# Kernel optimization log

Hardware: AMD Instinct MI355X
Metric: run time of the kernel (lower is better)

The kernel has to match this reference:

```python
import jax, jax.numpy as jnp
import numpy as np

B, T, NN = 128, 128, 8          # batch, time_window, nodes per graph (hardcoded in source)
N = B * T * NN                  # 131072 flattened node rows
F_IN, C = 32, 64                # node_features, spatial_features
E = 1_048_576                   # edges (avg degree 8)
EPS = 1e-5


def _gcn(x, src, dst, W, b):
    # PyG GCNConv: h = D^{-1/2}(A+I)D^{-1/2} X W + b, self-loops added, symmetric norm
    h = x @ W                                           # [N, C]
    loop = jnp.arange(N, dtype=src.dtype)
    s = jnp.concatenate([src, loop])
    d = jnp.concatenate([dst, loop])
    deg = jax.ops.segment_sum(jnp.ones_like(s, dtype=h.dtype), d, num_segments=N)
    dinv = jax.lax.rsqrt(deg)                           # deg >= 1 due to self loops
    msg = h[s] * (dinv[s] * dinv[d])[:, None]           # gather + scale
    out = jax.ops.segment_sum(msg, d, num_segments=N)   # scatter-add
    return out + b


def _conv2d(x, w, b, pad_w):
    y = jax.lax.conv_general_dilated(
        x, w, window_strides=(1, 1), padding=[(0, 0), (pad_w, pad_w)],
        dimension_numbers=("NCHW", "OIHW", "NCHW"))
    return y + b[None, :, None, None]


def _bn_relu(x, g, beta):
    # BatchNorm2d in training mode: batch statistics, biased variance
    mu = x.mean(axis=(0, 2, 3), keepdims=True)
    var = x.var(axis=(0, 2, 3), keepdims=True)
    y = (x - mu) * jax.lax.rsqrt(var + EPS)
    return jax.nn.relu(y * g[None, :, None, None] + beta[None, :, None, None])


def _layer(x, src, dst, gw, gb, tw, tb, bg, bb, ow, ob):
    h = _gcn(x, src, dst, gw, gb)                       # [N, C]
    h = h.reshape(B, T, NN, -1).transpose(0, 3, 2, 1)   # [B, C, NN, T]
    h = _conv2d(h, tw, tb, 1)                           # (1,3) temporal conv, pad (0,1)
    h = _bn_relu(h, bg, bb)
    h = _conv2d(h, ow, ob, 0)                           # 1x1 conv (squeeze() is a no-op here)
    h = jnp.tanh(h)
    return h.reshape(-1, h.shape[1])                    # faithful to x.view(-1, x.shape[1])


def setup_inputs() -> dict:
    key = jax.random.key(0)
    ks = jax.random.split(key, 20)
    p = lambda k, shape: (jax.random.normal(k, shape, jnp.float32) * 0.05)
    inp = {
        "x": jax.random.normal(ks[0], (N, F_IN), jnp.float32),
        "edge_index": jax.random.randint(ks[1], (2, E), 0, N, jnp.int32),
        "gcn1_w": p(ks[2], (F_IN, C)), "gcn1_b": jnp.zeros((C,), jnp.float32),
        "t1_w": p(ks[3], (C, C, 1, 3)), "t1_b": jnp.zeros((C,), jnp.float32),
        "bn1_g": jnp.ones((C,), jnp.float32), "bn1_b": jnp.zeros((C,), jnp.float32),
        "o1_w": p(ks[4], (C, C, 1, 1)), "o1_b": jnp.zeros((C,), jnp.float32),
        "gcn2_w": p(ks[5], (C, C)), "gcn2_b": jnp.zeros((C,), jnp.float32),
        "t2_w": p(ks[6], (C, C, 1, 3)), "t2_b": jnp.zeros((C,), jnp.float32),
        "bn2_g": jnp.ones((C,), jnp.float32), "bn2_b": jnp.zeros((C,), jnp.float32),
        "o2_w": p(ks[7], (C, C, 1, 1)), "o2_b": jnp.zeros((C,), jnp.float32),
        "reg_w": p(ks[8], (C, 8)), "reg_b": jnp.zeros((8,), jnp.float32),
    }
    return inp


def reference(x, edge_index, gcn1_w, gcn1_b, t1_w, t1_b, bn1_g, bn1_b, o1_w, o1_b,
              gcn2_w, gcn2_b, t2_w, t2_b, bn2_g, bn2_b, o2_w, o2_b, reg_w, reg_b):
    src, dst = edge_index[0], edge_index[1]
    h = _layer(x, src, dst, gcn1_w, gcn1_b, t1_w, t1_b, bn1_g, bn1_b, o1_w, o1_b)
    h = _layer(h, src, dst, gcn2_w, gcn2_b, t2_w, t2_b, bn2_g, bn2_b, o2_w, o2_b)
    h = h @ reg_w + reg_b                                # [N, 8]
    h = h.reshape(B, T, NN, -1)
    return h.mean(axis=(1, 3))                           # [B, NN] = [128, 8]
```

## Files before the change

kernel.cpp:

```cpp
#include <hip/hip_runtime.h>
#include <stdint.h>

typedef unsigned short u16;
typedef __attribute__((ext_vector_type(8))) short bf16x8;
typedef __attribute__((ext_vector_type(4))) float f32x4;

static const int N_NODES = 131072;
static const int N_EDGES = 1048576;

__device__ __forceinline__ float u2f(u16 u){
  union{uint32_t i; float f;} w; w.i = ((uint32_t)u)<<16; return w.f;
}
__device__ __forceinline__ u16 f2u(float f){
  union{float f; uint32_t u;} v; v.f=f;
  uint32_t u=v.u;
  u += 0x7fff + ((u>>16)&1);
  return (u16)(u>>16);
}
__device__ __forceinline__ float bits2f(uint32_t b){
  union{uint32_t i; float f;} w; w.i = b; return w.f;
}
__device__ __forceinline__ float ldmix(const void* p, int i, int isbf){
  return isbf ? u2f(((const u16*)p)[i]) : ((const float*)p)[i];
}
__device__ __forceinline__ float ftanh(float x){
  float ax = fabsf(x);
  float e  = __expf(ax + ax);
  float r  = 1.f - __fdividef(2.f, e + 1.f);
  return copysignf(r, x);
}

__global__ __launch_bounds__(256) void k_hist(const int* __restrict__ dst, int* __restrict__ H,
                                              const uint32_t* __restrict__ x, int* __restrict__ flag,
                                              float* __restrict__ stats1, float* __restrict__ stats2,
                                              float* __restrict__ zacc){
  __shared__ int h[256];
  __shared__ int dcnt;
  int tid = threadIdx.x;
  h[tid] = 0;
  if (blockIdx.x == 0){
    if (tid == 0) dcnt = 0;
    for (int i=tid; i<512; i+=256){ stats1[i] = 0.f; stats2[i] = 0.f; }
    for (int i=tid; i<1024; i+=256) zacc[i] = 0.f;
  }
  __syncthreads();
  if (blockIdx.x == 0){
    uint32_t e = (x[tid]>>7) & 0xFFu;
    int ok = (e >= 0x6Fu && e <= 0x85u) ? 1 : 0;
    unsigned long long m = __ballot(ok);
    if ((tid & 63) == 0) atomicAdd(&dcnt, (int)__popcll(m));
    __syncthreads();
    if (tid == 0) *flag = (dcnt >= 128) ? 1 : 0;
  }
  int base = blockIdx.x*4096;
  #pragma unroll
  for (int i=0;i<16;i++){
    int e2 = base + i*256 + tid;
    atomicAdd(&h[(dst[e2] & (N_NODES-1))>>9], 1);
  }
  __syncthreads();
  H[blockIdx.x*256 + tid] = h[tid];
}

__device__ __forceinline__ void wcomb_one(int Kin, const void* gW, const void* gb, const void* tw,
                                          int isbf, u16* Wtb, float* braw, int r, int co){
  if (r < 3*Kin){
    int k = r / Kin, j = r - (r/Kin)*Kin;
    float acc = 0.f;
    for (int c=0; c<64; c++)
      acc += ldmix(gW, j*64+c, isbf) * ldmix(tw, co*192 + c*3 + k, isbf);
    Wtb[co*(3*Kin) + r] = f2u(acc);
  } else {
    int k = r - 3*Kin;
    float acc = 0.f;
    for (int c=0; c<64; c++)
      acc += ldmix(gb, c, isbf) * ldmix(tw, co*192 + c*3 + k, isbf);
    braw[k*64 + co] = acc;
  }
}

__global__ __launch_bounds__(256) void k_colscan_w(const int* __restrict__ H, int* __restrict__ P,
                                                   int* __restrict__ bt,
                                                   const void* __restrict__ g1w, const void* __restrict__ g1b,
                                                   const void* __restrict__ t1w,
                                                   const void* __restrict__ g2w, const void* __restrict__ g2b,
                                                   const void* __restrict__ t2w,
                                                   const void* __restrict__ o1w, const void* __restrict__ o2w,
                                                   const int* __restrict__ flag,
                                                   u16* __restrict__ Wtb1, float* __restrict__ braw1,
                                                   u16* __restrict__ Wtb2, float* __restrict__ braw2,
                                                   u16* __restrict__ owb1, u16* __restrict__ owb2){
  int tid = threadIdx.x;
  if (blockIdx.x < 256){
    __shared__ int sc[256];
    int b = blockIdx.x;
    int v = H[tid*256 + b];
    sc[tid] = v; __syncthreads();
    for (int d=1; d<256; d<<=1){
      int o = (tid>=d) ? sc[tid-d] : 0; __syncthreads();
      sc[tid] += o; __syncthreads();
    }
    P[tid*256 + b] = sc[tid] - v;
    if (tid==255) bt[b] = sc[255];
  } else {
    int isbf = *flag;
    int r = (blockIdx.x - 256)*4 + (tid>>6);
    int co = tid & 63;
    if (r >= 422) return;
    if (r < 99) wcomb_one(32, g1w, g1b, t1w, isbf, Wtb1, braw1, r, co);
    else if (r < 294) wcomb_one(64, g2w, g2b, t2w, isbf, Wtb2, braw2, r-99, co);
    else if (r < 358){
      int row = r - 294;
      owb1[row*64 + co] = f2u(ldmix(o1w, row*64 + co, isbf));
    } else {
      int row = r - 358;
      owb2[row*64 + co] = f2u(ldmix(o2w, row*64 + co, isbf));
    }
  }
}

__global__ __launch_bounds__(256) void k_scatter2(const int* __restrict__ src, const int* __restrict__ dst,
                                                  const int* __restrict__ P, const int* __restrict__ bt,
                                                  uint32_t* __restrict__ ebuf){
  __shared__ int cu[256], sc[256];
  int tid = threadIdx.x;
  int v = bt[tid];
  sc[tid] = v; __syncthreads();
  for (int d=1; d<256; d<<=1){
    int o = (tid>=d) ? sc[tid-d] : 0; __syncthreads();
    sc[tid] += o; __syncthreads();
  }
  cu[tid] = (sc[tid] - v) + P[blockIdx.x*256 + tid];
  __syncthreads();
  int base = blockIdx.x*4096;
  #pragma unroll
  for (int i=0;i<16;i++){
    int e = base + i*256 + tid;
    int s = src[e] & (N_NODES-1);
    int d = dst[e] & (N_NODES-1);
    int pos = atomicAdd(&cu[d>>9], 1);
    ebuf[pos] = (uint32_t)s | ((uint32_t)(d & 511) << 17);
  }
}

__global__ __launch_bounds__(512) void k_bsort2(const uint32_t* __restrict__ ebuf, const int* __restrict__ bt,
                                                const void* __restrict__ x, const int* __restrict__ flag,
                                                int* __restrict__ adj, int* __restrict__ offs,
                                                int* __restrict__ deg, float* __restrict__ dinv,
                                                u16* __restrict__ Bout, int* __restrict__ perm){
  __shared__ uint32_t ein[5120], outs[5120];
  __shared__ int hist[512], sc[512], cu[512];
  __shared__ int sct[256];
  __shared__ float dv[512];
  __shared__ int dh2[64], dsc[64];
  int b = blockIdx.x, tid = threadIdx.x;
  if (tid < 256){ sct[tid] = bt[tid]; }
  __syncthreads();
  for (int d=1; d<256; d<<=1){
    int o = (tid < 256 && tid>=d) ? sct[tid-d] : 0; __syncthreads();
    if (tid < 256) sct[tid] += o; __syncthreads();
  }
  int lo = sct[b] - bt[b], hi = sct[b];
  int cnt = hi - lo; if (cnt > 5120) cnt = 5120; if (cnt < 0) cnt = 0;
  hist[tid] = 0;
  __syncthreads();
  for (int i=tid; i<cnt; i+=512){
    uint32_t p = ebuf[lo+i];
    ein[i] = p;
    atomicAdd(&hist[(p>>17)&511], 1);
  }
  __syncthreads();
  sc[tid] = hist[tid];
  __syncthreads();
  for (int d=1; d<512; d<<=1){
    int v = (tid>=d) ? sc[tid-d] : 0;
    __syncthreads();
    sc[tid] += v;
    __syncthreads();
  }
  {
    int ex = sc[tid] - hist[tid];
    int node = b*512 + tid;
    offs[node] = lo + ex;
    deg[node]  = hist[tid];
    float rs = rsqrtf((float)hist[tid] + 1.0f);
    dinv[node] = rs;
    dv[tid] = rs;
    cu[tid] = ex;
  }
  __syncthreads();
  for (int i=tid; i<cnt; i+=512){
    uint32_t p = ein[i];
    int pos = atomicAdd(&cu[(p>>17)&511], 1);
    outs[pos] = p & 0x1FFFFu;
  }
  __syncthreads();
  if (tid < 64) dh2[tid] = 0;
  __syncthreads();
  int mybin = min(hist[tid], 63);
  atomicAdd(&dh2[mybin], 1);
  __syncthreads();
  if (tid == 0){
    int s = 0;
    for (int i=0;i<64;i++){ int c = dh2[i]; dsc[i] = s; s += c; }
  }
  __syncthreads();
  {
    int rank = atomicAdd(&dsc[mybin], 1);
    perm[(b<<9) + rank] = (b<<9) + tid;
  }
  for (int i=tid; i<cnt; i+=512) adj[lo+i] = (int)outs[i];
  int isbf = *flag;
  {
    uint32_t* Bd = (uint32_t*)Bout;
    for (int u=tid; u<8192; u+=512){
      int nl = u>>4, jd = u&15;
      int half = ((b<<9) + nl)*16 + jd;
      float x0, x1;
      if (isbf){
        uint32_t pr = ((const uint32_t*)x)[half];
        x0 = bits2f(pr<<16); x1 = bits2f(pr & 0xFFFF0000u);
      } else {
        float2 f2 = ((const float2*)x)[half];
        x0 = f2.x; x1 = f2.y;
      }
      float d = dv[nl];
      Bd[half] = (uint32_t)f2u(x0*d) | ((uint32_t)f2u(x1*d) << 16);
    }
  }
}

__device__ __forceinline__ void acc16(uint4 a, float* acc){
  acc[0] += bits2f(a.x<<16); acc[1] += bits2f(a.x&0xFFFF0000u);
  acc[2] += bits2f(a.y<<16); acc[3] += bits2f(a.y&0xFFFF0000u);
  acc[4] += bits2f(a.z<<16); acc[5] += bits2f(a.z&0xFFFF0000u);
  acc[6] += bits2f(a.w<<16); acc[7] += bits2f(a.w&0xFFFF0000u);
}
template<int F>
__global__ __launch_bounds__(256) void k_aggp2(const u16* __restrict__ Xs, const int* __restrict__ perm,
                                               const int* __restrict__ adj, const int* __restrict__ offs,
                                               const int* __restrict__ deg, const float* __restrict__ dinv,
                                               u16* __restrict__ out){
  constexpr int CH  = F/8;
  constexpr int GPW = 64/CH;
  int tid = threadIdx.x;
  int wv = tid>>6, lane = tid&63;
  int g = lane / CH;
  int k = lane % CH;
  int n = perm[blockIdx.x*(4*GPW) + wv*GPW + g];
  int o = offs[n] & (N_EDGES-1);
  int cnt = min(deg[n], 8192);
  const uint4* X4 = (const uint4*)Xs;
  uint4 sv = X4[(size_t)n*CH + k];
  float acc[8] = {0,0,0,0,0,0,0,0};
  acc16(sv, acc);
  int e = 0;
  for (; e+8 <= cnt; e += 8){
    int i0 = adj[o+e+0] & (N_NODES-1);
    int i1 = adj[o+e+1] & (N_NODES-1);
    int i2 = adj[o+e+2] & (N_NODES-1);
    int i3 = adj[o+e+3] & (N_NODES-1);
    int i4 = adj[o+e+4] & (N_NODES-1);
    int i5 = adj[o+e+5] & (N_NODES-1);
    int i6 = adj[o+e+6] & (N_NODES-1);
    int i7 = adj[o+e+7] & (N_NODES-1);
    uint4 a0 = X4[(size_t)i0*CH + k];
    uint4 a1 = X4[(size_t)i1*CH + k];
    uint4 a2 = X4[(size_t)i2*CH + k];
    uint4 a3 = X4[(size_t)i3*CH + k];
    uint4 a4 = X4[(size_t)i4*CH + k];
    uint4 a5 = X4[(size_t)i5*CH + k];
    uint4 a6 = X4[(size_t)i6*CH + k];
    uint4 a7 = X4[(size_t)i7*CH + k];
    acc16(a0, acc); acc16(a1, acc); acc16(a2, acc); acc16(a3, acc);
    acc16(a4, acc); acc16(a5, acc); acc16(a6, acc); acc16(a7, acc);
  }
  if (e+4 <= cnt){
    int i0 = adj[o+e+0] & (N_NODES-1);
    int i1 = adj[o+e+1] & (N_NODES-1);
    int i2 = adj[o+e+2] & (N_NODES-1);
    int i3 = adj[o+e+3] & (N_NODES-1);
    uint4 a0 = X4[(size_t)i0*CH + k];
    uint4 a1 = X4[(size_t)i1*CH + k];
    uint4 a2 = X4[(size_t)i2*CH + k];
    uint4 a3 = X4[(size_t)i3*CH + k];
    acc16(a0, acc); acc16(a1, acc); acc16(a2, acc); acc16(a3, acc);
    e += 4;
  }
  for (; e < cnt; e++){
    int s = adj[o+e] & (N_NODES-1);
    uint4 a = X4[(size_t)s*CH + k];
    acc16(a, acc);
  }
  float dv = dinv[n];
  uint4 r;
  r.x = (uint32_t)f2u(acc[0]*dv) | ((uint32_t)f2u(acc[1]*dv) << 16);
  r.y = (uint32_t)f2u(acc[2]*dv) | ((uint32_t)f2u(acc[3]*dv) << 16);
  r.z = (uint32_t)f2u(acc[4]*dv) | ((uint32_t)f2u(acc[5]*dv) << 16);
  r.w = (uint32_t)f2u(acc[6]*dv) | ((uint32_t)f2u(acc[7]*dv) << 16);
  ((uint4*)out)[(size_t)n*CH + k] = r;
}

template<int Kin>
__global__ __launch_bounds__(256) void k_tconv3(const u16* __restrict__ A, const u16* __restrict__ Wtb,
                                                const float* __restrict__ braw, const void* __restrict__ tb,
                                                const int* __restrict__ flag, u16* __restrict__ out,
                                                float* __restrict__ stats){
  constexpr int K  = 3*Kin;
  constexpr int SA = Kin + 8;
  constexpr int JH = Kin/2;
  constexpr int JL = (Kin==64) ? 5 : 4;
  __shared__ alignas(16) u16 At[66*SA];
  __shared__ float ball[64], bs0[64], bs2[64];
  __shared__ float wsum[4][64], wsum2[4][64];

  int isbf = *flag;
  int bid = blockIdx.x;
  int b = bid>>4, rem = bid&15, v = rem>>1, th = rem&1;
  const int tid = threadIdx.x;

  if (tid < 64){
    float b0=braw[tid], b1=braw[64+tid], b2=braw[128+tid];
    ball[tid] = ldmix(tb, tid, isbf) + b0 + b1 + b2;
    bs0[tid] = b0; bs2[tid] = b2;
  }
  {
    uint32_t* Ad = (uint32_t*)At;
    const uint32_t* Ag = (const uint32_t*)A;
    for (int u=tid; u<66*JH; u+=256){
      int ls = u >> JL, jd = u & (JH-1);
      int t = th*64 + ls - 1;
      uint32_t pack = 0;
      if (t >= 0 && t < 128)
        pack = Ag[((((b*128+t)*8+v))*Kin >> 1) + jd];
      Ad[ls*(SA/2) + jd] = pack;
    }
  }
  __syncthreads();

  int wv_ = tid >> 6, lane = tid & 63;
  int q = lane >> 4, l16 = lane & 15;
  int ltb0 = wv_ * 16;

  f32x4 acc[4];
  #pragma unroll
  for (int nt=0; nt<4; nt++) acc[nt] = (f32x4){0.f,0.f,0.f,0.f};

  #pragma unroll
  for (int s=0; s<K/32; s++){
    int kk = (32*s)/Kin;
    int j0 = 32*s - kk*Kin;
    int col = j0 + q*8;
    bf16x8 afr = *(const bf16x8*)&At[(ltb0 + l16 + kk)*SA + col];
    bf16x8 bfr[4];
    #pragma unroll
    for (int nt=0; nt<4; nt++){
      int co = nt*16 + l16;
      bfr[nt] = *(const bf16x8*)&Wtb[co*K + 32*s + q*8];
    }
    #pragma unroll
    for (int nt=0; nt<4; nt++)
      acc[nt] = __builtin_amdgcn_mfma_f32_16x16x32_bf16(afr, bfr[nt], acc[nt], 0, 0, 0);
  }

  float ls_[4] = {0,0,0,0}, ls2_[4] = {0,0,0,0};
  #pragma unroll
  for (int r=0; r<4; r++){
    int t = th*64 + ltb0 + q*4 + r;
    int base = (((b*128+t)*8+v)) << 6;
    #pragma unroll
    for (int nt=0; nt<4; nt++){
      int co = nt*16 + l16;
      float val = acc[nt][r] + ball[co];
      if (t == 0)   val -= bs0[co];
      if (t == 127) val -= bs2[co];
      out[base + co] = f2u(val);
      ls_[nt] += val; ls2_[nt] += val*val;
    }
  }
  #pragma unroll
  for (int nt=0; nt<4; nt++){
    ls_[nt]  += __shfl_xor(ls_[nt], 16);  ls_[nt]  += __shfl_xor(ls_[nt], 32);
    ls2_[nt] += __shfl_xor(ls2_[nt], 16); ls2_[nt] += __shfl_xor(ls2_[nt], 32);
  }
  if (q == 0){
    #pragma unroll
    for (int nt=0; nt<4; nt++){
      wsum[wv_][nt*16 + l16]  = ls_[nt];
      wsum2[wv_][nt*16 + l16] = ls2_[nt];
    }
  }
  __syncthreads();
  if (tid < 64){
    float a = wsum[0][tid]+wsum[1][tid]+wsum[2][tid]+wsum[3][tid];
    float a2 = wsum2[0][tid]+wsum2[1][tid]+wsum2[2][tid]+wsum2[3][tid];
    int bank = (bid & 3) * 128;
    atomicAdd(&stats[bank + tid], a);
    atomicAdd(&stats[bank + 64 + tid], a2);
  }
}

template<bool FINAL>
__global__ __launch_bounds__(256) void k_bnfuse3(const u16* __restrict__ X, const float* __restrict__ stats,
                                                 const void* __restrict__ gam, const void* __restrict__ bet,
                                                 const u16* __restrict__ owb, const void* __restrict__ ob,
                                                 const int* __restrict__ flag, const float* __restrict__ presc,
                                                 u16* __restrict__ out16,
                                                 float* __restrict__ zacc, const void* __restrict__ rw){
  constexpr int SA = 72;
  __shared__ alignas(16) u16 Yl[64*SA];
  __shared__ float kk[64], bsh[64], obs[64];
  __shared__ float rw_s[64];
  __shared__ float wred[4];
  int isbf = *flag;
  int bid = blockIdx.x;
  int b = bid>>4, rem = bid&15, v = rem>>1, th = rem&1;
  const int tid = threadIdx.x;
  const float invM = 1.0f/131072.0f;

  if (tid < 64){
    int ci = tid;
    float s1 = stats[ci] + stats[128+ci] + stats[256+ci] + stats[384+ci];
    float s2 = stats[64+ci] + stats[192+ci] + stats[320+ci] + stats[448+ci];
    float mu = s1*invM;
    float var = s2*invM - mu*mu;
    float rs = rsqrtf(fmaxf(var, 0.f) + 1e-5f);
    float kv = rs*ldmix(gam, ci, isbf);
    kk[ci] = kv;
    bsh[ci] = ldmix(bet, ci, isbf) - mu*kv;
    obs[ci] = ldmix(ob, ci, isbf);
    if (FINAL){
      float s = 0.f;
      #pragma unroll
      for (int f=0; f<8; f++) s += ldmix(rw, ci*8 + f, isbf);
      rw_s[ci] = s;
    }
  }
  __syncthreads();
  {
    uint32_t* Yd = (uint32_t*)Yl;
    const uint32_t* Xg = (const uint32_t*)X;
    for (int u=tid; u<64*32; u+=256){
      int lt = u>>5, jd = u&31;
      int ci = jd<<1;
      int t = th*64 + lt;
      int rowbase = (((b*128+t)*8+v)) << 6;
      uint32_t pr = Xg[(rowbase>>1) + jd];
      float x0 = bits2f(pr<<16);
      float x1 = bits2f(pr & 0xFFFF0000u);
      float y0 = fmaxf(x0*kk[ci] + bsh[ci], 0.f);
      float y1 = fmaxf(x1*kk[ci+1] + bsh[ci+1], 0.f);
      Yd[lt*(SA/2) + jd] = (uint32_t)f2u(y0) | ((uint32_t)f2u(y1) << 16);
    }
  }
  __syncthreads();

  int wv_ = tid >> 6, lane = tid & 63;
  int q = lane >> 4, l16 = lane & 15;
  int ltb0 = wv_ * 16;

  f32x4 acc[4];
  #pragma unroll
  for (int nt=0; nt<4; nt++) acc[nt] = (f32x4){0.f,0.f,0.f,0.f};

  #pragma unroll
  for (int s=0; s<2; s++){
    int col = 32*s + q*8;
    bf16x8 afr = *(const bf16x8*)&Yl[(ltb0 + l16)*SA + col];
    bf16x8 bfr[4];
    #pragma unroll
    for (int nt=0; nt<4; nt++){
      int co = nt*16 + l16;
      bfr[nt] = *(const bf16x8*)&owb[co*64 + col];
    }
    #pragma unroll
    for (int nt=0; nt<4; nt++)
      acc[nt] = __builtin_amdgcn_mfma_f32_16x16x32_bf16(afr, bfr[nt], acc[nt], 0, 0, 0);
  }

  __syncthreads();
  #pragma unroll
  for (int r=0; r<4; r++){
    int lt = ltb0 + q*4 + r;
    #pragma unroll
    for (int nt=0; nt<4; nt++){
      int co = nt*16 + l16;
      Yl[lt*SA + co] = f2u(acc[nt][r] + obs[co]);
    }
  }
  __syncthreads();
  if (!FINAL){
    for (int u=tid; u<4096; u+=256){
      int l = u & 63;
      int co = u >> 6;
      float z = ftanh(u2f(Yl[l*SA + co]));
      int r = (b<<10) + (co<<4) + (v<<1) + th;
      if (presc) z *= presc[r];
      out16[(r<<6) + l] = f2u(z);
    }
  } else {
    float zsum = 0.f;
    for (int u=tid; u<4096; u+=256){
      int l = u & 63;
      int co = u >> 6;
      float z = ftanh(u2f(Yl[l*SA + co]));
      zsum += z * rw_s[l];
    }
    for (int off=32; off; off>>=1) zsum += __shfl_down(zsum, off);
    if (lane == 0) wred[wv_] = zsum;
    __syncthreads();
    if (tid == 0){
      int base = (b<<3) + ((v&3)<<1) + th;
      atomicAdd(&zacc[base], wred[0] + wred[1] + wred[2] + wred[3]);
    }
  }
}

__global__ __launch_bounds__(256) void k_fin2(const float* __restrict__ zacc, const void* __restrict__ rb,
                                              const int* __restrict__ flag, void* __restrict__ out){
  int i = blockIdx.x*256 + threadIdx.x;
  if (i >= 1024) return;
  int isbf = *flag;
  float rbs = 0.f;
  #pragma unroll
  for (int f=0; f<8; f++) rbs += ldmix(rb, f, isbf);
  float val = zacc[i]*(1.0f/1024.0f) + rbs*0.125f;
  if (isbf) ((u16*)out)[i] = f2u(val);
  else      ((float*)out)[i] = val;
}

extern "C" void kernel_launch(void* const* d_in, const int* in_sizes, int n_in,
                              void* d_out, int out_size, void* d_ws, size_t ws_size,
                              hipStream_t stream){
  (void)in_sizes; (void)n_in; (void)out_size; (void)ws_size;
  char* p = (char*)d_ws;
  auto alloc = [&](size_t bytes){ void* r = (void*)p; p += (bytes + 255) & ~(size_t)255; return r; };
  u16*   U1   = (u16*)  alloc(sizeof(u16)*(size_t)N_NODES*64);
  u16*   U2   = (u16*)  alloc(sizeof(u16)*(size_t)N_NODES*64);
  u16*   C16  = (u16*)  alloc(sizeof(u16)*(size_t)N_NODES*64);
  int*   deg  = (int*)  alloc(sizeof(int)*N_NODES);
  float* dinv = (float*)alloc(sizeof(float)*N_NODES);
  int*   offs = (int*)  alloc(sizeof(int)*N_NODES);
  int*   adj  = (int*)  alloc(sizeof(int)*N_EDGES);
  int*   perm = (int*)  alloc(sizeof(int)*N_NODES);
  int*   H    = (int*)  alloc(sizeof(int)*256*256);
  int*   P    = (int*)  alloc(sizeof(int)*256*256);
  int*   bt   = (int*)  alloc(sizeof(int)*256);
  float* stats1=(float*)alloc(sizeof(float)*512);
  float* stats2=(float*)alloc(sizeof(float)*512);
  int*   flag = (int*)  alloc(sizeof(int)*64);
  u16*   Wtb1 = (u16*)  alloc(sizeof(u16)*96*64);
  float* braw1= (float*)alloc(sizeof(float)*192);
  u16*   Wtb2 = (u16*)  alloc(sizeof(u16)*192*64);
  float* braw2= (float*)alloc(sizeof(float)*192);
  u16*   owb1 = (u16*)  alloc(sizeof(u16)*64*64);
  u16*   owb2 = (u16*)  alloc(sizeof(u16)*64*64);
  float* zacc = (float*)alloc(sizeof(float)*1024);
  uint32_t* ebuf = (uint32_t*)C16;
  u16* Bs16 = U1;
  u16* A16  = U1 + (size_t)N_NODES*32;
  u16* D16  = U1;
  u16* E16  = U2;

  const void* x   = d_in[0];
  const int* edge = (const int*)d_in[1];
  const void* g1w = d_in[2];  const void* g1b = d_in[3];
  const void* t1w = d_in[4];  const void* t1b = d_in[5];
  const void* bn1g= d_in[6];  const void* bn1b= d_in[7];
  const void* o1w = d_in[8];  const void* o1b = d_in[9];
  const void* g2w = d_in[10]; const void* g2b = d_in[11];
  const void* t2w = d_in[12]; const void* t2b = d_in[13];
  const void* bn2g= d_in[14]; const void* bn2b= d_in[15];
  const void* o2w = d_in[16]; const void* o2b = d_in[17];
  const void* rw  = d_in[18]; const void* rb  = d_in[19];
  const int* src = edge;
  const int* dst = edge + N_EDGES;

  k_hist     <<<256, 256, 0, stream>>>(dst, H, (const uint32_t*)x, flag, stats1, stats2, zacc);
  k_colscan_w<<<362, 256, 0, stream>>>(H, P, bt, g1w, g1b, t1w, g2w, g2b, t2w, o1w, o2w, flag,
                                       Wtb1, braw1, Wtb2, braw2, owb1, owb2);
  k_scatter2 <<<256, 256, 0, stream>>>(src, dst, P, bt, ebuf);
  k_bsort2   <<<256, 512, 0, stream>>>(ebuf, bt, x, flag, adj, offs, deg, dinv, Bs16, perm);

  k_aggp2<32>  <<<N_NODES/64, 256, 0, stream>>>(Bs16, perm, adj, offs, deg, dinv, A16);
  k_tconv3<32> <<<2048, 256, 0, stream>>>(A16, Wtb1, braw1, t1b, flag, C16, stats1);
  k_bnfuse3<false><<<2048, 256, 0, stream>>>(C16, stats1, bn1g, bn1b, owb1, o1b, flag, dinv, D16,
                                             (float*)nullptr, (const void*)nullptr);

  k_aggp2<64>  <<<N_NODES/32, 256, 0, stream>>>(D16, perm, adj, offs, deg, dinv, E16);
  k_tconv3<64> <<<2048, 256, 0, stream>>>(E16, Wtb2, braw2, t2b, flag, C16, stats2);
  k_bnfuse3<true><<<2048, 256, 0, stream>>>(C16, stats2, bn2g, bn2b, owb2, o2b, flag, (const float*)nullptr,
                                            (u16*)nullptr, zacc, rw);
  k_fin2<<<4, 256, 0, stream>>>(zacc, rb, flag, d_out);
}
```

Before: 296.3 us.

## Fuse GCN neighbor aggregation into temporal conv kernel and drop degree-sorted permutation

The separate sparse aggregation kernel is removed. Each temporal-conv block now gathers and aggregates its own 66 time rows (64 plus a halo) straight into shared memory before the MFMA conv. This avoids writing the aggregated features to global memory and reading them back, and it removes the degree-binned node permutation built in the sort kernel. In exchange, the 2 halo rows per block are aggregated twice, and load balancing across lanes with different degrees is lost because nodes are no longer grouped by degree.

```diff
diff --git a/kernel.cpp b/kernel.cpp
--- a/kernel.cpp
+++ b/kernel.cpp
@@ -147,12 +147,11 @@
                                                 const void* __restrict__ x, const int* __restrict__ flag,
                                                 int* __restrict__ adj, int* __restrict__ offs,
                                                 int* __restrict__ deg, float* __restrict__ dinv,
-                                                u16* __restrict__ Bout, int* __restrict__ perm){
+                                                u16* __restrict__ Bout){
   __shared__ uint32_t ein[5120], outs[5120];
   __shared__ int hist[512], sc[512], cu[512];
   __shared__ int sct[256];
   __shared__ float dv[512];
-  __shared__ int dh2[64], dsc[64];
   int b = blockIdx.x, tid = threadIdx.x;
   if (tid < 256){ sct[tid] = bt[tid]; }
   __syncthreads();
@@ -195,20 +194,6 @@
     outs[pos] = p & 0x1FFFFu;
   }
   __syncthreads();
-  if (tid < 64) dh2[tid] = 0;
-  __syncthreads();
-  int mybin = min(hist[tid], 63);
-  atomicAdd(&dh2[mybin], 1);
-  __syncthreads();
-  if (tid == 0){
-    int s = 0;
-    for (int i=0;i<64;i++){ int c = dh2[i]; dsc[i] = s; s += c; }
-  }
-  __syncthreads();
-  {
-    int rank = atomicAdd(&dsc[mybin], 1);
-    perm[(b<<9) + rank] = (b<<9) + tid;
-  }
   for (int i=tid; i<cnt; i+=512) adj[lo+i] = (int)outs[i];
   int isbf = *flag;
   {
@@ -236,80 +221,17 @@
   acc[4] += bits2f(a.z<<16); acc[5] += bits2f(a.z&0xFFFF0000u);
   acc[6] += bits2f(a.w<<16); acc[7] += bits2f(a.w&0xFFFF0000u);
 }
-template<int F>
-__global__ __launch_bounds__(256) void k_aggp2(const u16* __restrict__ Xs, const int* __restrict__ perm,
-                                               const int* __restrict__ adj, const int* __restrict__ offs,
-                                               const int* __restrict__ deg, const float* __restrict__ dinv,
-                                               u16* __restrict__ out){
-  constexpr int CH  = F/8;
+
+template<int Kin>
+__global__ __launch_bounds__(256) void k_gconv(
+    const u16* __restrict__ Xs, const int* __restrict__ adj, const int* __restrict__ offs,
+    const int* __restrict__ deg, const float* __restrict__ dinv,
+    const u16* __restrict__ Wtb, const float* __restrict__ braw, const void* __restrict__ tb,
+    const int* __restrict__ flag, u16* __restrict__ out, float* __restrict__ stats){
+  constexpr int K   = 3*Kin;
+  constexpr int SA  = Kin + 8;
+  constexpr int CH  = Kin/8;
   constexpr int GPW = 64/CH;
-  int tid = threadIdx.x;
-  int wv = tid>>6, lane = tid&63;
-  int g = lane / CH;
-  int k = lane % CH;
-  int n = perm[blockIdx.x*(4*GPW) + wv*GPW + g];
-  int o = offs[n] & (N_EDGES-1);
-  int cnt = min(deg[n], 8192);
-  const uint4* X4 = (const uint4*)Xs;
-  uint4 sv = X4[(size_t)n*CH + k];
-  float acc[8] = {0,0,0,0,0,0,0,0};
-  acc16(sv, acc);
-  int e = 0;
-  for (; e+8 <= cnt; e += 8){
-    int i0 = adj[o+e+0] & (N_NODES-1);
-    int i1 = adj[o+e+1] & (N_NODES-1);
-    int i2 = adj[o+e+2] & (N_NODES-1);
-    int i3 = adj[o+e+3] & (N_NODES-1);
-    int i4 = adj[o+e+4] & (N_NODES-1);
-    int i5 = adj[o+e+5] & (N_NODES-1);
-    int i6 = adj[o+e+6] & (N_NODES-1);
-    int i7 = adj[o+e+7] & (N_NODES-1);
-    uint4 a0 = X4[(size_t)i0*CH + k];
-    uint4 a1 = X4[(size_t)i1*CH + k];
-    uint4 a2 = X4[(size_t)i2*CH + k];
-    uint4 a3 = X4[(size_t)i3*CH + k];
-    uint4 a4 = X4[(size_t)i4*CH + k];
-    uint4 a5 = X4[(size_t)i5*CH + k];
-    uint4 a6 = X4[(size_t)i6*CH + k];
-    uint4 a7 = X4[(size_t)i7*CH + k];
-    acc16(a0, acc); acc16(a1, acc); acc16(a2, acc); acc16(a3, acc);
-    acc16(a4, acc); acc16(a5, acc); acc16(a6, acc); acc16(a7, acc);
-  }
-  if (e+4 <= cnt){
-    int i0 = adj[o+e+0] & (N_NODES-1);
-    int i1 = adj[o+e+1] & (N_NODES-1);
-    int i2 = adj[o+e+2] & (N_NODES-1);
-    int i3 = adj[o+e+3] & (N_NODES-1);
-    uint4 a0 = X4[(size_t)i0*CH + k];
-    uint4 a1 = X4[(size_t)i1*CH + k];
-    uint4 a2 = X4[(size_t)i2*CH + k];
-    uint4 a3 = X4[(size_t)i3*CH + k];
-    acc16(a0, acc); acc16(a1, acc); acc16(a2, acc); acc16(a3, acc);
-    e += 4;
-  }
-  for (; e < cnt; e++){
-    int s = adj[o+e] & (N_NODES-1);
-    uint4 a = X4[(size_t)s*CH + k];
-    acc16(a, acc);
-  }
-  float dv = dinv[n];
-  uint4 r;
-  r.x = (uint32_t)f2u(acc[0]*dv) | ((uint32_t)f2u(acc[1]*dv) << 16);
-  r.y = (uint32_t)f2u(acc[2]*dv) | ((uint32_t)f2u(acc[3]*dv) << 16);
-  r.z = (uint32_t)f2u(acc[4]*dv) | ((uint32_t)f2u(acc[5]*dv) << 16);
-  r.w = (uint32_t)f2u(acc[6]*dv) | ((uint32_t)f2u(acc[7]*dv) << 16);
-  ((uint4*)out)[(size_t)n*CH + k] = r;
-}
-
-template<int Kin>
-__global__ __launch_bounds__(256) void k_tconv3(const u16* __restrict__ A, const u16* __restrict__ Wtb,
-                                                const float* __restrict__ braw, const void* __restrict__ tb,
-                                                const int* __restrict__ flag, u16* __restrict__ out,
-                                                float* __restrict__ stats){
-  constexpr int K  = 3*Kin;
-  constexpr int SA = Kin + 8;
-  constexpr int JH = Kin/2;
-  constexpr int JL = (Kin==64) ? 5 : 4;
   __shared__ alignas(16) u16 At[66*SA];
   __shared__ float ball[64], bs0[64], bs2[64];
   __shared__ float wsum[4][64], wsum2[4][64];
@@ -318,40 +240,84 @@
   int bid = blockIdx.x;
   int b = bid>>4, rem = bid&15, v = rem>>1, th = rem&1;
   const int tid = threadIdx.x;
+  int wv_ = tid >> 6, lane = tid & 63;
+  int q = lane >> 4, l16 = lane & 15;
+  int ltb0 = wv_ * 16;
+  int g = lane / CH, kch = lane % CH;
+  const uint4* X4 = (const uint4*)Xs;
 
   if (tid < 64){
     float b0=braw[tid], b1=braw[64+tid], b2=braw[128+tid];
     ball[tid] = ldmix(tb, tid, isbf) + b0 + b1 + b2;
     bs0[tid] = b0; bs2[tid] = b2;
   }
-  {
-    uint32_t* Ad = (uint32_t*)At;
-    const uint32_t* Ag = (const uint32_t*)A;
-    for (int u=tid; u<66*JH; u+=256){
-      int ls = u >> JL, jd = u & (JH-1);
-      int t = th*64 + ls - 1;
-      uint32_t pack = 0;
-      if (t >= 0 && t < 128)
-        pack = Ag[((((b*128+t)*8+v))*Kin >> 1) + jd];
-      Ad[ls*(SA/2) + jd] = pack;
-    }
-  }
-  __syncthreads();
-
-  int wv_ = tid >> 6, lane = tid & 63;
-  int q = lane >> 4, l16 = lane & 15;
-  int ltb0 = wv_ * 16;
-
-  f32x4 acc[4];
-  #pragma unroll
-  for (int nt=0; nt<4; nt++) acc[nt] = (f32x4){0.f,0.f,0.f,0.f};
-
+
+  for (int row = wv_*GPW + g; row < 66; row += 4*GPW){
+    int t = th*64 + row - 1;
+    uint4 rv = {0,0,0,0};
+    if (t >= 0 && t < 128){
+      int n = (b*128 + t)*8 + v;
+      int o = offs[n] & (N_EDGES-1);
+      int cnt = min(deg[n], 8192);
+      float dvv = dinv[n];
+      float acc[8] = {0,0,0,0,0,0,0,0};
+      acc16(X4[(size_t)n*CH + kch], acc);
+      int e = 0;
+      for (; e+8 <= cnt; e += 8){
+        int i0 = adj[o+e+0] & (N_NODES-1);
+        int i1 = adj[o+e+1] & (N_NODES-1);
+        int i2 = adj[o+e+2] & (N_NODES-1);
+        int i3 = adj[o+e+3] & (N_NODES-1);
+        int i4 = adj[o+e+4] & (N_NODES-1);
+        int i5 = adj[o+e+5] & (N_NODES-1);
+        int i6 = adj[o+e+6] & (N_NODES-1);
+        int i7 = adj[o+e+7] & (N_NODES-1);
+        uint4 a0 = X4[(size_t)i0*CH + kch];
+        uint4 a1 = X4[(size_t)i1*CH + kch];
+        uint4 a2 = X4[(size_t)i2*CH + kch];
+        uint4 a3 = X4[(size_t)i3*CH + kch];
+        uint4 a4 = X4[(size_t)i4*CH + kch];
+        uint4 a5 = X4[(size_t)i5*CH + kch];
+        uint4 a6 = X4[(size_t)i6*CH + kch];
+        uint4 a7 = X4[(size_t)i7*CH + kch];
+        acc16(a0, acc); acc16(a1, acc); acc16(a2, acc); acc16(a3, acc);
+        acc16(a4, acc); acc16(a5, acc); acc16(a6, acc); acc16(a7, acc);
+      }
+      if (e+4 <= cnt){
+        int i0 = adj[o+e+0] & (N_NODES-1);
+        int i1 = adj[o+e+1] & (N_NODES-1);
+        int i2 = adj[o+e+2] & (N_NODES-1);
+        int i3 = adj[o+e+3] & (N_NODES-1);
+        uint4 a0 = X4[(size_t)i0*CH + kch];
+        uint4 a1 = X4[(size_t)i1*CH + kch];
+        uint4 a2 = X4[(size_t)i2*CH + kch];
+        uint4 a3 = X4[(size_t)i3*CH + kch];
+        acc16(a0, acc); acc16(a1, acc); acc16(a2, acc); acc16(a3, acc);
+        e += 4;
+      }
+      for (; e < cnt; e++){
+        int s = adj[o+e] & (N_NODES-1);
+        uint4 a = X4[(size_t)s*CH + kch];
+        acc16(a, acc);
+      }
+      rv.x = (uint32_t)f2u(acc[0]*dvv) | ((uint32_t)f2u(acc[1]*dvv) << 16);
+      rv.y = (uint32_t)f2u(acc[2]*dvv) | ((uint32_t)f2u(acc[3]*dvv) << 16);
+      rv.z = (uint32_t)f2u(acc[4]*dvv) | ((uint32_t)f2u(acc[5]*dvv) << 16);
+      rv.w = (uint32_t)f2u(acc[6]*dvv) | ((uint32_t)f2u(acc[7]*dvv) << 16);
+    }
+    *(uint4*)&At[row*SA + kch*8] = rv;
+  }
+  __syncthreads();
+
+  f32x4 acc4[4];
+  #pragma unroll
+  for (int nt=0; nt<4; nt++) acc4[nt] = (f32x4){0.f,0.f,0.f,0.f};
   #pragma unroll
   for (int s=0; s<K/32; s++){
-    int kk = (32*s)/Kin;
-    int j0 = 32*s - kk*Kin;
+    int kk2 = (32*s)/Kin;
+    int j0 = 32*s - kk2*Kin;
     int col = j0 + q*8;
-    bf16x8 afr = *(const bf16x8*)&At[(ltb0 + l16 + kk)*SA + col];
+    bf16x8 afr = *(const bf16x8*)&At[(ltb0 + l16 + kk2)*SA + col];
     bf16x8 bfr[4];
     #pragma unroll
     for (int nt=0; nt<4; nt++){
@@ -360,7 +326,7 @@
     }
     #pragma unroll
     for (int nt=0; nt<4; nt++)
-      acc[nt] = __builtin_amdgcn_mfma_f32_16x16x32_bf16(afr, bfr[nt], acc[nt], 0, 0, 0);
+      acc4[nt] = __builtin_amdgcn_mfma_f32_16x16x32_bf16(afr, bfr[nt], acc4[nt], 0, 0, 0);
   }
 
   float ls_[4] = {0,0,0,0}, ls2_[4] = {0,0,0,0};
@@ -371,7 +337,7 @@
     #pragma unroll
     for (int nt=0; nt<4; nt++){
       int co = nt*16 + l16;
-      float val = acc[nt][r] + ball[co];
+      float val = acc4[nt][r] + ball[co];
       if (t == 0)   val -= bs0[co];
       if (t == 127) val -= bs2[co];
       out[base + co] = f2u(val);
@@ -542,7 +508,6 @@
   float* dinv = (float*)alloc(sizeof(float)*N_NODES);
   int*   offs = (int*)  alloc(sizeof(int)*N_NODES);
   int*   adj  = (int*)  alloc(sizeof(int)*N_EDGES);
-  int*   perm = (int*)  alloc(sizeof(int)*N_NODES);
   int*   H    = (int*)  alloc(sizeof(int)*256*256);
   int*   P    = (int*)  alloc(sizeof(int)*256*256);
   int*   bt   = (int*)  alloc(sizeof(int)*256);
@@ -558,9 +523,8 @@
   float* zacc = (float*)alloc(sizeof(float)*1024);
   uint32_t* ebuf = (uint32_t*)C16;
   u16* Bs16 = U1;
-  u16* A16  = U1 + (size_t)N_NODES*32;
   u16* D16  = U1;
-  u16* E16  = U2;
+  (void)U2;
 
   const void* x   = d_in[0];
   const int* edge = (const int*)d_in[1];
@@ -580,15 +544,13 @@
   k_colscan_w<<<362, 256, 0, stream>>>(H, P, bt, g1w, g1b, t1w, g2w, g2b, t2w, o1w, o2w, flag,
                                        Wtb1, braw1, Wtb2, braw2, owb1, owb2);
   k_scatter2 <<<256, 256, 0, stream>>>(src, dst, P, bt, ebuf);
-  k_bsort2   <<<256, 512, 0, stream>>>(ebuf, bt, x, flag, adj, offs, deg, dinv, Bs16, perm);
-
-  k_aggp2<32>  <<<N_NODES/64, 256, 0, stream>>>(Bs16, perm, adj, offs, deg, dinv, A16);
-  k_tconv3<32> <<<2048, 256, 0, stream>>>(A16, Wtb1, braw1, t1b, flag, C16, stats1);
+  k_bsort2   <<<256, 512, 0, stream>>>(ebuf, bt, x, flag, adj, offs, deg, dinv, Bs16);
+
+  k_gconv<32> <<<2048, 256, 0, stream>>>(Bs16, adj, offs, deg, dinv, Wtb1, braw1, t1b, flag, C16, stats1);
   k_bnfuse3<false><<<2048, 256, 0, stream>>>(C16, stats1, bn1g, bn1b, owb1, o1b, flag, dinv, D16,
                                              (float*)nullptr, (const void*)nullptr);
 
-  k_aggp2<64>  <<<N_NODES/32, 256, 0, stream>>>(D16, perm, adj, offs, deg, dinv, E16);
-  k_tconv3<64> <<<2048, 256, 0, stream>>>(E16, Wtb2, braw2, t2b, flag, C16, stats2);
+  k_gconv<64> <<<2048, 256, 0, stream>>>(D16, adj, offs, deg, dinv, Wtb2, braw2, t2b, flag, C16, stats2);
   k_bnfuse3<true><<<2048, 256, 0, stream>>>(C16, stats2, bn2g, bn2b, owb2, o2b, flag, (const float*)nullptr,
                                             (u16*)nullptr, zacc, rw);
   k_fin2<<<4, 256, 0, stream>>>(zacc, rb, flag, d_out);
```

Result: faster. 274.2 us (-7.5%).
